# Kernel optimization log

Hardware: AMD Instinct MI355X
Metric: run time of the kernel (lower is better)

The kernel has to match this reference:

```python
import jax, jax.numpy as jnp
import numpy as np

B, F, BOND, NFREQ, NOUT, INIT_STD = 16384, 256, 16, 4, 1, 0.1


def setup_inputs() -> dict:
    key = jax.random.key(0)
    ks = jax.random.split(key, 10)
    x = jax.random.uniform(ks[0], (B, F), dtype=jnp.float32)
    inp = {"x": x, "frequency_min": jnp.array(1.0, dtype=jnp.float32)}
    d_in = 1 + 2 * NFREQ  # physical leg dim = 9
    n, level = F, 0
    while n > 1:
        n2 = n // 2
        d_out = NOUT if n == 2 else BOND
        # stack all same-level node tensors: [n_pairs, d_left, d_right, d_out]
        inp[f"W{level}"] = jax.random.normal(ks[level + 1], (n2, d_in, d_in, d_out), dtype=jnp.float32) * INIT_STD
        d_in, n, level = d_out, n2, level + 1
    return inp


def reference(x, frequency_min, W0, W1, W2, W3, W4, W5, W6, W7):
    Ws = [W0, W1, W2, W3, W4, W5, W6, W7]
    nfreq = (W0.shape[1] - 1) // 2
    # Fourier feature map: [B, F, 1+2*nfreq]
    xs = (x * frequency_min)[..., None]
    freqs = jnp.arange(1, nfreq + 1, dtype=x.dtype)
    feats = jnp.concatenate(
        [jnp.ones_like(xs), jnp.sin(xs * freqs), jnp.cos(xs * freqs)], axis=-1
    )
    nodes = feats  # [B, n_nodes, d]
    for W in Ws:
        left = nodes[:, 0::2]   # [B, n/2, d]
        right = nodes[:, 1::2]  # [B, n/2, d]
        # batched pairwise bilinear contraction over all nodes of one level
        nodes = jnp.einsum('bni,nijd,bnj->bnd', left, W, right)
    return nodes[:, 0, :]  # [B, NOUT]
```

## Files before the change

kernel.cpp:

```cpp
#include <hip/hip_runtime.h>
#include <math.h>

#define BTOT 16384

typedef __attribute__((ext_vector_type(8))) short s16x8;
typedef __attribute__((ext_vector_type(4))) float f32x4;
typedef __attribute__((ext_vector_type(4))) uint u32x4;
typedef __attribute__((ext_vector_type(2))) float f32x2;
typedef __attribute__((ext_vector_type(2))) uint u32x2;

#define OFF0 0u
#define OFF1 655360u
#define OFF2 1179648u
#define OFF3 1441792u
#define OFF4 1572864u
#define OFF5 1638400u
#define OFF6 1671168u
#define OFF7 1687552u

__device__ __forceinline__ ushort rtn_bf16(float x) {
  uint u = __builtin_bit_cast(uint, x);
  uint r = u + 0x7fffu + ((u >> 16) & 1u);
  return (ushort)(r >> 16);
}

__global__ __launch_bounds__(256) void wprep_kernel(
    const float* __restrict__ W0, const float* __restrict__ W1,
    const float* __restrict__ W2, const float* __restrict__ W3,
    const float* __restrict__ W4, const float* __restrict__ W5,
    const float* __restrict__ W6, const float* __restrict__ W7,
    ushort* __restrict__ U) {
  int blk = blockIdx.x;
  const float* Wsrc; ushort* dst; int ktN, din; bool dout1 = false;
  if (blk < 128)      { Wsrc = W0 + blk * 1296;         dst = U + OFF0 + (size_t)blk * 5120;         ktN = 5; din = 9;  }
  else if (blk < 192) { Wsrc = W1 + (blk - 128) * 4096; dst = U + OFF1 + (size_t)(blk - 128) * 8192; ktN = 8; din = 16; }
  else if (blk < 224) { Wsrc = W2 + (blk - 192) * 4096; dst = U + OFF2 + (size_t)(blk - 192) * 8192; ktN = 8; din = 16; }
  else if (blk < 240) { Wsrc = W3 + (blk - 224) * 4096; dst = U + OFF3 + (size_t)(blk - 224) * 8192; ktN = 8; din = 16; }
  else if (blk < 248) { Wsrc = W4 + (blk - 240) * 4096; dst = U + OFF4 + (size_t)(blk - 240) * 8192; ktN = 8; din = 16; }
  else if (blk < 252) { Wsrc = W5 + (blk - 248) * 4096; dst = U + OFF5 + (size_t)(blk - 248) * 8192; ktN = 8; din = 16; }
  else if (blk < 254) { Wsrc = W6 + (blk - 252) * 4096; dst = U + OFF6 + (size_t)(blk - 252) * 8192; ktN = 8; din = 16; }
  else                { Wsrc = W7;                      dst = U + OFF7;                              ktN = 8; din = 16; dout1 = true; }
  int entries = ktN * 512;
  for (int e = threadIdx.x; e < entries; e += 256) {
    int kt = e >> 9, l = (e >> 3) & 63, jv = e & 7;
    int k = kt * 32 + ((l >> 4) << 3) + jv;
    int i = k >> 4, j = k & 15, n = l & 15;
    float w;
    if (dout1) w = (n == 0) ? Wsrc[i * 16 + j] : 0.f;
    else       w = (i < din && j < din) ? Wsrc[(i * din + j) * 16 + n] : 0.f;
    uint u = __builtin_bit_cast(uint, w);
    uint h = u & 0xffff0000u;
    dst[e] = (ushort)(h >> 16);
    dst[entries + e] = rtn_bf16(w - __builtin_bit_cast(float, h));
  }
}

__device__ __forceinline__ f32x4 split3(float li, const f32x2* rf2,
                                        s16x8 wh, s16x8 wl, f32x4 acc) {
  const f32x2 li2 = {li, li};
  u32x4 hv, lv;
#pragma unroll
  for (int jp = 0; jp < 4; ++jp) {
    f32x2 p2 = li2 * rf2[jp];
    u32x2 u2 = __builtin_bit_cast(u32x2, p2);
    u32x2 hb = u2 & 0xffff0000u;
    f32x2 h2 = __builtin_bit_cast(f32x2, hb);
    f32x2 q2 = __builtin_elementwise_fma(li2, rf2[jp], -h2);
    u32x2 uq = __builtin_bit_cast(u32x2, q2);
    hv[jp] = __builtin_amdgcn_perm(u2.y, u2.x, 0x07060302u);
    lv[jp] = __builtin_amdgcn_perm(uq.y, uq.x, 0x07060302u);
  }
  s16x8 ahi = __builtin_bit_cast(s16x8, hv);
  s16x8 alo = __builtin_bit_cast(s16x8, lv);
  acc = __builtin_amdgcn_mfma_f32_16x16x32_bf16(ahi, wh, acc, 0, 0, 0);
  acc = __builtin_amdgcn_mfma_f32_16x16x32_bf16(alo, wh, acc, 0, 0, 0);
  acc = __builtin_amdgcn_mfma_f32_16x16x32_bf16(ahi, wl, acc, 0, 0, 0);
  return acc;
}

template <int KTN, bool L0M>
__device__ __forceinline__ f32x4 mfma_core(const float* Lcol, const float* Rcol,
                                           const int ld, const ushort* __restrict__ Wf,
                                           int lane) {
  const int g = lane >> 4;
  const int j0 = (g & 1) * 8, gh = g >> 1;
  const float* Lg = Lcol + gh * ld;
  float lf[KTN];
#pragma unroll
  for (int i = 0; i < KTN; ++i) lf[i] = Lg[2 * i * ld];
  f32x2 rf2[4];
#pragma unroll
  for (int j = 0; j < 8; ++j) {
    float v = (L0M && (j0 + j >= 9)) ? 0.f : Rcol[(j0 + j) * ld];
    rf2[j >> 1][j & 1] = v;
  }
  f32x4 acc = {0.f, 0.f, 0.f, 0.f};
  const int entries = KTN * 512;
#pragma unroll
  for (int kt = 0; kt < KTN; ++kt) {
    const s16x8 wh = *(const s16x8*)&Wf[(kt * 64 + lane) * 8];
    const s16x8 wl = *(const s16x8*)&Wf[entries + (kt * 64 + lane) * 8];
    acc = split3(lf[kt], rf2, wh, wl, acc);
  }
  return acc;
}

#define LDF 67

__device__ __forceinline__ void feats_col(float xv, float* Fb, int col) {
  float s1 = __sinf(xv), c1 = __cosf(xv);
  Fb[0 * LDF + col] = 1.f; Fb[1 * LDF + col] = s1; Fb[5 * LDF + col] = c1;
  float sk = s1, ck = c1;
#pragma unroll
  for (int k = 2; k <= 4; ++k) {
    float sn = s1 * ck + c1 * sk, cn = c1 * ck - s1 * sk;
    sk = sn; ck = cn;
    Fb[k * LDF + col] = sk; Fb[(4 + k) * LDF + col] = ck;
  }
}

__global__ __launch_bounds__(256, 4) void ttn_front_kernel(
    const float* __restrict__ x, const float* __restrict__ fminp,
    const ushort* __restrict__ U, float* __restrict__ s1out) {
  __shared__ float F0[10 * LDF], F1[10 * LDF];
  __shared__ float A0[16 * LDF], B0[16 * LDF];
  __shared__ float A1[16 * LDF], B1[16 * LDF];
  __shared__ float A2[16 * LDF], B2[16 * LDF];

  const int tid = threadIdx.x;
  const int lane = tid & 63, w = tid >> 6;
  const int m = lane & 15, g = lane >> 4;
  const int bl = w * 16 + m;
  const int b0 = blockIdx.x * 64;
  const int s = blockIdx.y;
  const float fmin = fminp[0];

  if (lane < 32) {
    int col = w * 16 + (lane & 15);
    ((lane >> 4) ? F1 : F0)[9 * LDF + col] = 0.f;
  }

  const float* xw = x + (size_t)(b0 + w * 16 + (lane & 15)) * 256 + s * 16;
  float* outG = s1out + (size_t)(s * 16) * BTOT + b0;

  auto storeL = [&](f32x4 a, float* Out) {
#pragma unroll
    for (int r = 0; r < 4; ++r) Out[m * LDF + w * 16 + g * 4 + r] = a[r];
  };

  for (int t = 0; t < 8; ++t) {
    if (lane < 32) {
      int side = lane >> 4;
      float xv = xw[2 * t + side] * fmin;
      feats_col(xv, side ? F1 : F0, w * 16 + (lane & 15));
    }
    f32x4 a = mfma_core<5, true>(&F0[bl], &F1[bl], LDF,
                                 U + OFF0 + (size_t)(8 * s + t) * 5120, lane);
    storeL(a, (t & 1) ? B0 : A0);
    if (t & 1) {
      f32x4 c1 = mfma_core<8, false>(&A0[bl], &B0[bl], LDF,
                                     U + OFF1 + (size_t)(4 * s + (t >> 1)) * 8192, lane);
      storeL(c1, ((t >> 1) & 1) ? B1 : A1);
      if ((t & 3) == 3) {
        f32x4 c2 = mfma_core<8, false>(&A1[bl], &B1[bl], LDF,
                                       U + OFF2 + (size_t)(2 * s + (t >> 2)) * 8192, lane);
        storeL(c2, ((t >> 2) & 1) ? B2 : A2);
        if (t == 7) {
          f32x4 c3 = mfma_core<8, false>(&A2[bl], &B2[bl], LDF,
                                         U + OFF3 + (size_t)s * 8192, lane);
#pragma unroll
          for (int r = 0; r < 4; ++r)
            outG[(size_t)m * BTOT + w * 16 + g * 4 + r] = c3[r];
        }
      }
    }
  }
}

__global__ __launch_bounds__(128) void ttn_back_kernel(
    const float* __restrict__ s1, const ushort* __restrict__ U,
    float* __restrict__ out) {
  __shared__ float P[2][2][16 * 17];
  __shared__ float S[4][16 * 17];
  const int tid = threadIdx.x;
  const int lane = tid & 63, w = tid >> 6;
  const int m = lane & 15, g = lane >> 4;
  const int b0 = blockIdx.x * 16;

  auto storeC = [&](f32x4 a, float* Buf) {
#pragma unroll
    for (int r = 0; r < 4; ++r) Buf[m * 17 + g * 4 + r] = a[r];
  };

#pragma unroll
  for (int h = 0; h < 2; ++h) {
    const int n0 = 4 * w + 2 * h;
#pragma unroll
    for (int p = 0; p < 2; ++p) {
      const int n = n0 + p;
      f32x4 a = mfma_core<8, false>(&s1[(size_t)(32 * n) * BTOT + b0 + m],
                                    &s1[(size_t)(32 * n + 16) * BTOT + b0 + m],
                                    BTOT, U + OFF4 + (size_t)n * 8192, lane);
      storeC(a, P[w][p]);
    }
    f32x4 a5 = mfma_core<8, false>(&P[w][0][m], &P[w][1][m], 17,
                                   U + OFF5 + (size_t)(2 * w + h) * 8192, lane);
    storeC(a5, S[2 * w + h]);
  }
  __syncthreads();

  {
    f32x4 a6 = mfma_core<8, false>(&S[2 * w][m], &S[2 * w + 1][m], 17,
                                   U + OFF6 + (size_t)w * 8192, lane);
    storeC(a6, S[2 * w]);
  }
  __syncthreads();

  if (w == 0) {
    f32x4 a7 = mfma_core<8, false>(&S[0][m], &S[2][m], 17, U + OFF7, lane);
    if (m == 0) {
#pragma unroll
      for (int r = 0; r < 4; ++r) out[b0 + g * 4 + r] = a7[r];
    }
  }
}

extern "C" void kernel_launch(void* const* d_in, const int* in_sizes, int n_in,
                              void* d_out, int out_size, void* d_ws, size_t ws_size,
                              hipStream_t stream) {
  const float* x    = (const float*)d_in[0];
  const float* fmin = (const float*)d_in[1];
  const float* W0   = (const float*)d_in[2];
  const float* W1   = (const float*)d_in[3];
  const float* W2   = (const float*)d_in[4];
  const float* W3   = (const float*)d_in[5];
  const float* W4   = (const float*)d_in[6];
  const float* W5   = (const float*)d_in[7];
  const float* W6   = (const float*)d_in[8];
  const float* W7   = (const float*)d_in[9];
  float* out = (float*)d_out;

  ushort* U = (ushort*)d_ws;
  float* s1 = (float*)((char*)d_ws + (4u << 20));

  wprep_kernel<<<255, 256, 0, stream>>>(W0, W1, W2, W3, W4, W5, W6, W7, U);
  ttn_front_kernel<<<dim3(256, 16), 256, 0, stream>>>(x, fmin, U, s1);
  ttn_back_kernel<<<1024, 128, 0, stream>>>(s1, U, out);
}
```

Measured before the change: 238.6 us.

## Stage back-kernel inputs through LDS with coalesced loads and stage weight prep in shared memory

```diff
diff --git a/kernel.cpp b/kernel.cpp
--- a/kernel.cpp
+++ b/kernel.cpp
@@ -30,24 +30,27 @@
     const float* __restrict__ W4, const float* __restrict__ W5,
     const float* __restrict__ W6, const float* __restrict__ W7,
     ushort* __restrict__ U) {
+  __shared__ float WL[4096];
   int blk = blockIdx.x;
-  const float* Wsrc; ushort* dst; int ktN, din; bool dout1 = false;
-  if (blk < 128)      { Wsrc = W0 + blk * 1296;         dst = U + OFF0 + (size_t)blk * 5120;         ktN = 5; din = 9;  }
-  else if (blk < 192) { Wsrc = W1 + (blk - 128) * 4096; dst = U + OFF1 + (size_t)(blk - 128) * 8192; ktN = 8; din = 16; }
-  else if (blk < 224) { Wsrc = W2 + (blk - 192) * 4096; dst = U + OFF2 + (size_t)(blk - 192) * 8192; ktN = 8; din = 16; }
-  else if (blk < 240) { Wsrc = W3 + (blk - 224) * 4096; dst = U + OFF3 + (size_t)(blk - 224) * 8192; ktN = 8; din = 16; }
-  else if (blk < 248) { Wsrc = W4 + (blk - 240) * 4096; dst = U + OFF4 + (size_t)(blk - 240) * 8192; ktN = 8; din = 16; }
-  else if (blk < 252) { Wsrc = W5 + (blk - 248) * 4096; dst = U + OFF5 + (size_t)(blk - 248) * 8192; ktN = 8; din = 16; }
-  else if (blk < 254) { Wsrc = W6 + (blk - 252) * 4096; dst = U + OFF6 + (size_t)(blk - 252) * 8192; ktN = 8; din = 16; }
-  else                { Wsrc = W7;                      dst = U + OFF7;                              ktN = 8; din = 16; dout1 = true; }
+  const float* Wsrc; ushort* dst; int ktN, din, nsrc; bool dout1 = false;
+  if (blk < 128)      { Wsrc = W0 + blk * 1296;         dst = U + OFF0 + (size_t)blk * 5120;         ktN = 5; din = 9;  nsrc = 1296; }
+  else if (blk < 192) { Wsrc = W1 + (blk - 128) * 4096; dst = U + OFF1 + (size_t)(blk - 128) * 8192; ktN = 8; din = 16; nsrc = 4096; }
+  else if (blk < 224) { Wsrc = W2 + (blk - 192) * 4096; dst = U + OFF2 + (size_t)(blk - 192) * 8192; ktN = 8; din = 16; nsrc = 4096; }
+  else if (blk < 240) { Wsrc = W3 + (blk - 224) * 4096; dst = U + OFF3 + (size_t)(blk - 224) * 8192; ktN = 8; din = 16; nsrc = 4096; }
+  else if (blk < 248) { Wsrc = W4 + (blk - 240) * 4096; dst = U + OFF4 + (size_t)(blk - 240) * 8192; ktN = 8; din = 16; nsrc = 4096; }
+  else if (blk < 252) { Wsrc = W5 + (blk - 248) * 4096; dst = U + OFF5 + (size_t)(blk - 248) * 8192; ktN = 8; din = 16; nsrc = 4096; }
+  else if (blk < 254) { Wsrc = W6 + (blk - 252) * 4096; dst = U + OFF6 + (size_t)(blk - 252) * 8192; ktN = 8; din = 16; nsrc = 4096; }
+  else                { Wsrc = W7;                      dst = U + OFF7;                              ktN = 8; din = 16; nsrc = 256; dout1 = true; }
+  for (int i = threadIdx.x; i < nsrc; i += 256) WL[i] = Wsrc[i];
+  __syncthreads();
   int entries = ktN * 512;
   for (int e = threadIdx.x; e < entries; e += 256) {
     int kt = e >> 9, l = (e >> 3) & 63, jv = e & 7;
     int k = kt * 32 + ((l >> 4) << 3) + jv;
     int i = k >> 4, j = k & 15, n = l & 15;
     float w;
-    if (dout1) w = (n == 0) ? Wsrc[i * 16 + j] : 0.f;
-    else       w = (i < din && j < din) ? Wsrc[(i * din + j) * 16 + n] : 0.f;
+    if (dout1) w = (n == 0) ? WL[i * 16 + j] : 0.f;
+    else       w = (i < din && j < din) ? WL[(i * din + j) * 16 + n] : 0.f;
     uint u = __builtin_bit_cast(uint, w);
     uint h = u & 0xffff0000u;
     dst[e] = (ushort)(h >> 16);
@@ -87,7 +90,8 @@
   const float* Lg = Lcol + gh * ld;
   float lf[KTN];
 #pragma unroll
-  for (int i = 0; i < KTN; ++i) lf[i] = Lg[2 * i * ld];
+  for (int i = 0; i < KTN; ++i)
+    lf[i] = (L0M && (2 * i + gh > 8)) ? 0.f : Lg[2 * i * ld];
   f32x2 rf2[4];
 #pragma unroll
   for (int j = 0; j < 8; ++j) {
@@ -122,7 +126,7 @@
 __global__ __launch_bounds__(256, 4) void ttn_front_kernel(
     const float* __restrict__ x, const float* __restrict__ fminp,
     const ushort* __restrict__ U, float* __restrict__ s1out) {
-  __shared__ float F0[10 * LDF], F1[10 * LDF];
+  __shared__ float F0[9 * LDF], F1[9 * LDF];
   __shared__ float A0[16 * LDF], B0[16 * LDF];
   __shared__ float A1[16 * LDF], B1[16 * LDF];
   __shared__ float A2[16 * LDF], B2[16 * LDF];
@@ -134,11 +138,6 @@
   const int b0 = blockIdx.x * 64;
   const int s = blockIdx.y;
   const float fmin = fminp[0];
-
-  if (lane < 32) {
-    int col = w * 16 + (lane & 15);
-    ((lane >> 4) ? F1 : F0)[9 * LDF + col] = 0.f;
-  }
 
   const float* xw = x + (size_t)(b0 + w * 16 + (lane & 15)) * 256 + s * 16;
   float* outG = s1out + (size_t)(s * 16) * BTOT + b0;
@@ -177,13 +176,13 @@
   }
 }
 
-__global__ __launch_bounds__(128) void ttn_back_kernel(
+__global__ __launch_bounds__(512) void ttn_back_kernel(
     const float* __restrict__ s1, const ushort* __restrict__ U,
     float* __restrict__ out) {
-  __shared__ float P[2][2][16 * 17];
-  __shared__ float S[4][16 * 17];
+  __shared__ float T[256 * 17];
+  __shared__ float P[8][16 * 17];
   const int tid = threadIdx.x;
-  const int lane = tid & 63, w = tid >> 6;
+  const int lane = tid & 63, v = tid >> 6;
   const int m = lane & 15, g = lane >> 4;
   const int b0 = blockIdx.x * 16;
 
@@ -193,34 +192,42 @@
   };
 
 #pragma unroll
-  for (int h = 0; h < 2; ++h) {
-    const int n0 = 4 * w + 2 * h;
-#pragma unroll
-    for (int p = 0; p < 2; ++p) {
-      const int n = n0 + p;
-      f32x4 a = mfma_core<8, false>(&s1[(size_t)(32 * n) * BTOT + b0 + m],
-                                    &s1[(size_t)(32 * n + 16) * BTOT + b0 + m],
-                                    BTOT, U + OFF4 + (size_t)n * 8192, lane);
-      storeC(a, P[w][p]);
-    }
-    f32x4 a5 = mfma_core<8, false>(&P[w][0][m], &P[w][1][m], 17,
-                                   U + OFF5 + (size_t)(2 * w + h) * 8192, lane);
-    storeC(a5, S[2 * w + h]);
+  for (int it = 0; it < 2; ++it) {
+    int idx = it * 512 + tid;
+    int r = idx >> 2, c4 = (idx & 3) * 4;
+    float4 vv = *(const float4*)&s1[(size_t)r * BTOT + b0 + c4];
+    T[r * 17 + c4 + 0] = vv.x; T[r * 17 + c4 + 1] = vv.y;
+    T[r * 17 + c4 + 2] = vv.z; T[r * 17 + c4 + 3] = vv.w;
   }
   __syncthreads();
 
   {
-    f32x4 a6 = mfma_core<8, false>(&S[2 * w][m], &S[2 * w + 1][m], 17,
-                                   U + OFF6 + (size_t)w * 8192, lane);
-    storeC(a6, S[2 * w]);
-  }
-  __syncthreads();
-
-  if (w == 0) {
-    f32x4 a7 = mfma_core<8, false>(&S[0][m], &S[2][m], 17, U + OFF7, lane);
+    f32x4 a = mfma_core<8, false>(&T[(32 * v) * 17 + m], &T[(32 * v + 16) * 17 + m],
+                                  17, U + OFF4 + (size_t)v * 8192, lane);
+    storeC(a, P[v]);
+  }
+  __syncthreads();
+
+  if (v < 4) {
+    f32x4 a = mfma_core<8, false>(&P[2 * v][m], &P[2 * v + 1][m], 17,
+                                  U + OFF5 + (size_t)v * 8192, lane);
+    storeC(a, &T[v * 16 * 17]);
+  }
+  __syncthreads();
+
+  if (v < 2) {
+    f32x4 a = mfma_core<8, false>(&T[(2 * v) * 16 * 17 + m],
+                                  &T[(2 * v + 1) * 16 * 17 + m], 17,
+                                  U + OFF6 + (size_t)v * 8192, lane);
+    storeC(a, P[v]);
+  }
+  __syncthreads();
+
+  if (v == 0) {
+    f32x4 a = mfma_core<8, false>(&P[0][m], &P[1][m], 17, U + OFF7, lane);
     if (m == 0) {
 #pragma unroll
-      for (int r = 0; r < 4; ++r) out[b0 + g * 4 + r] = a7[r];
+      for (int r = 0; r < 4; ++r) out[b0 + g * 4 + r] = a[r];
     }
   }
 }
@@ -245,5 +252,5 @@
 
   wprep_kernel<<<255, 256, 0, stream>>>(W0, W1, W2, W3, W4, W5, W6, W7, U);
   ttn_front_kernel<<<dim3(256, 16), 256, 0, stream>>>(x, fmin, U, s1);
-  ttn_back_kernel<<<1024, 128, 0, stream>>>(s1, U, out);
-}
+  ttn_back_kernel<<<1024, 512, 0, stream>>>(s1, U, out);
+}
```

After: 234.6 us, median of 2. No clear change (-1.7%).
